# Kernel tuning notes

Hardware: AMD Instinct MI355X
Metric: run time of the kernel (lower is better)

Reference implementation:

```python
import jax, jax.numpy as jnp
import numpy as np

D_MODEL = 1024
H = 16
D_K = D_MODEL // H  # 64
B, S = 2, 2048


def setup_inputs() -> dict:
    key = jax.random.key(0)
    ks = jax.random.split(key, 8)
    scale = 1.0 / np.sqrt(D_MODEL)
    return {
        "q": jax.random.normal(ks[0], (B, S, D_MODEL), dtype=jnp.float32),
        "k": jax.random.normal(ks[1], (B, S, D_MODEL), dtype=jnp.float32),
        "v": jax.random.normal(ks[2], (B, S, D_MODEL), dtype=jnp.float32),
        "W_q": jax.random.normal(ks[3], (H, D_MODEL, D_K), dtype=jnp.float32) * scale,
        "W_k": jax.random.normal(ks[4], (H, D_MODEL, D_K), dtype=jnp.float32) * scale,
        "W_v": jax.random.normal(ks[5], (H, D_MODEL, D_K), dtype=jnp.float32) * scale,
        "W_o": jax.random.normal(ks[6], (D_MODEL, H * D_K), dtype=jnp.float32) * scale,
        "b_o": jnp.zeros((D_MODEL,), dtype=jnp.float32),
    }


def reference(q, k, v, W_q, W_k, W_v, W_o, b_o):
    b, s, _ = q.shape
    h, _, d_k = W_q.shape
    inv_sqrt_dk = jnp.asarray(1.0 / np.sqrt(d_k), q.dtype)
    # per-head projections: [b, h, s, d_k]
    qh = jnp.einsum("bsd,hdk->bhsk", q, W_q)
    kh = jnp.einsum("bsd,hdk->bhsk", k, W_k)
    vh = jnp.einsum("bsd,hdk->bhsk", v, W_v)
    # scaled dot product attention
    scores = jnp.einsum("bhqk,bhsk->bhqs", qh, kh) * inv_sqrt_dk  # [b,h,S,S]
    attn = jax.nn.softmax(scores, axis=-1)
    ctx = jnp.einsum("bhqs,bhsk->bhqk", attn, vh)  # [b,h,S,d_k]
    # chunk over heads + concat along feature dim -> [b, S, h*d_k], head-major
    ctx = ctx.transpose(0, 2, 1, 3).reshape(b, s, h * d_k)
    # final linear
    return ctx @ W_o.T + b_o
```

## Files before the change

kernel.cpp:

```cpp
#include <hip/hip_runtime.h>
#include <cstdint>
#include <cstddef>


typedef unsigned short bf16_t;
typedef __attribute__((ext_vector_type(8))) short short8;
typedef __attribute__((ext_vector_type(4))) float f32x4;

__device__ __forceinline__ uint32_t fbits(float f) {
  union { float f; uint32_t u; } v; v.f = f; return v.u;
}
__device__ __forceinline__ bf16_t f2bf(float f) {
  uint32_t u = fbits(f);
  return (bf16_t)((u + 0x7FFFu + ((u >> 16) & 1u)) >> 16);
}
__device__ __forceinline__ uint32_t packbf2(float lo, float hi) {
  uint32_t a = fbits(hi) + 0x8000u;
  uint32_t b = fbits(lo) + 0x8000u;
  return __builtin_amdgcn_perm(a, b, 0x07060302u);
}
__device__ __forceinline__ int4 cvt8(f32x4 lo, f32x4 hi) {
  return make_int4((int)packbf2(lo.x, lo.y), (int)packbf2(lo.z, lo.w),
                   (int)packbf2(hi.x, hi.y), (int)packbf2(hi.z, hi.w));
}

__global__ void prep_kernel(const float* __restrict__ Wo,
                            const float* __restrict__ Wq, const float* __restrict__ Wk,
                            const float* __restrict__ Wv,
                            bf16_t* __restrict__ Woo,
                            bf16_t* __restrict__ Wtq, bf16_t* __restrict__ Wtk,
                            bf16_t* __restrict__ Wtv) {
  int blk = blockIdx.x;
  int tid = threadIdx.x;
  if (blk < 1024) {
    int i = blk * 256 + tid;
    f32x4 val = ((const f32x4*)Wo)[i];
    ushort4 o;
    o.x = f2bf(val.x); o.y = f2bf(val.y); o.z = f2bf(val.z); o.w = f2bf(val.w);
    ((ushort4*)Woo)[i] = o;
  } else {
    int blk2 = blk - 1024;
    int z = blk2 >> 9, t = blk2 & 511;
    const float* W = z == 0 ? Wq : z == 1 ? Wk : Wv;
    bf16_t* Wt = z == 0 ? Wtq : z == 1 ? Wtk : Wtv;
    int h = t >> 5, d0 = (t & 31) * 32;
    __shared__ float tile[32][65];
    const float* src = W + ((size_t)h << 16) + (size_t)d0 * 64;
    int d = tid >> 3;
#pragma unroll
    for (int j = 0; j < 2; j++) {
      int dk = (tid & 7) * 8 + j * 4;
      *(f32x4*)&tile[d][dk] = *(const f32x4*)(src + d * 64 + dk);
    }
    __syncthreads();
    int dk2 = tid >> 2, c = tid & 3;
    union { ushort s[8]; int4 v; } o;
#pragma unroll
    for (int j = 0; j < 8; j++) o.s[j] = f2bf(tile[c * 8 + j][dk2]);
    *(int4*)(Wt + (size_t)(h * 64 + dk2) * 1024 + d0 + c * 8) = o.v;
  }
}

__global__ __launch_bounds__(256) void gemm_proj_kernel(
    const float* __restrict__ A0, const float* __restrict__ A1, const float* __restrict__ A2,
    const bf16_t* __restrict__ B0, const bf16_t* __restrict__ B1, const bf16_t* __restrict__ B2,
    bf16_t* __restrict__ O0, bf16_t* __restrict__ O1, bf16_t* __restrict__ O2,
    float s0)
{
  const int bid = blockIdx.x;
  const int nIdx = bid / 96;
  const int g = bid - nIdx * 96;
  const int z = g % 3;
  const int m0 = (g / 3) * 128, n0 = nIdx * 128;

  const float* A   = z == 0 ? A0 : z == 1 ? A1 : A2;
  const bf16_t* Bt = z == 0 ? B0 : z == 1 ? B1 : B2;
  bf16_t* Cout     = z == 0 ? O0 : z == 1 ? O1 : O2;
  const float scale = z == 0 ? s0 : 1.0f;
  const int K = 1024;

  __shared__ alignas(16) bf16_t smem[18432];

  const int tid = threadIdx.x;
  const int lane = tid & 63, wave = tid >> 6;
  const int wm = wave >> 1, wn = wave & 1;
  const int quad = lane >> 4, l15 = lane & 15;

  f32x4 acc[4][4];
#pragma unroll
  for (int i = 0; i < 4; i++)
#pragma unroll
    for (int j = 0; j < 4; j++) acc[i][j] = (f32x4)0.0f;

  const int c0 = wave * 128 + lane;
  const int c1 = c0 + 64;
  const float*  pa0 = A  + (size_t)(m0 + (c0 >> 2)) * K + (c0 & 3) * 8;
  const float*  pa1 = A  + (size_t)(m0 + (c1 >> 2)) * K + (c1 & 3) * 8;
  const bf16_t* pb0 = Bt + (size_t)(n0 + (c0 >> 2)) * K + (c0 & 3) * 8;
  const bf16_t* pb1 = Bt + (size_t)(n0 + (c1 >> 2)) * K + (c1 & 3) * 8;
  const int s0a = c0 * 8, s1a = c1 * 8;

  f32x4 ra0l = *(const f32x4*)pa0, ra0h = *(const f32x4*)(pa0 + 4);
  f32x4 ra1l = *(const f32x4*)pa1, ra1h = *(const f32x4*)(pa1 + 4);
  int4 rb0 = *(const int4*)pb0;
  int4 rb1 = *(const int4*)pb1;
  *(int4*)(smem + s0a) = cvt8(ra0l, ra0h);
  *(int4*)(smem + s1a) = cvt8(ra1l, ra1h);
  *(int4*)(smem + 4096 + s0a) = rb0;
  *(int4*)(smem + 4096 + s1a) = rb1;
  __syncthreads();

  for (int it = 0; it < 32; ++it) {
    const int co = (it & 1) * 8192;
    if (it < 31) {
      const int ko = (it + 1) * 32;
      ra0l = *(const f32x4*)(pa0 + ko); ra0h = *(const f32x4*)(pa0 + ko + 4);
      ra1l = *(const f32x4*)(pa1 + ko); ra1h = *(const f32x4*)(pa1 + ko + 4);
      rb0 = *(const int4*)(pb0 + ko);
      rb1 = *(const int4*)(pb1 + ko);
    }

    short8 af[4], bfr[4];
#pragma unroll
    for (int mi = 0; mi < 4; mi++)
      af[mi] = *(const short8*)(smem + co + (wm * 64 + mi * 16 + l15) * 32 + quad * 8);
#pragma unroll
    for (int ni = 0; ni < 4; ni++)
      bfr[ni] = *(const short8*)(smem + co + 4096 + (wn * 64 + ni * 16 + l15) * 32 + quad * 8);
#pragma unroll
    for (int mi = 0; mi < 4; mi++)
#pragma unroll
      for (int ni = 0; ni < 4; ni++)
        acc[mi][ni] = __builtin_amdgcn_mfma_f32_16x16x32_bf16(af[mi], bfr[ni], acc[mi][ni], 0, 0, 0);

    if (it < 31) {
      const int no = ((it + 1) & 1) * 8192;
      *(int4*)(smem + no + s0a) = cvt8(ra0l, ra0h);
      *(int4*)(smem + no + s1a) = cvt8(ra1l, ra1h);
      *(int4*)(smem + no + 4096 + s0a) = rb0;
      *(int4*)(smem + no + 4096 + s1a) = rb1;
    }
    __syncthreads();
  }

  const int s0r = m0 & 2047, bb = m0 >> 11, hp = n0 >> 6;
  if (z < 2) {
    bf16_t* slot = smem + wn * 9216;
#pragma unroll
    for (int ni = 0; ni < 4; ni++)
#pragma unroll
      for (int mi = 0; mi < 4; mi++)
#pragma unroll
        for (int r = 0; r < 4; r++)
          slot[(wm * 64 + mi * 16 + quad * 4 + r) * 72 + ni * 16 + l15] =
              f2bf(acc[mi][ni][r] * scale);
    __syncthreads();
#pragma unroll
    for (int rd = 0; rd < 8; ++rd) {
      int idx = rd * 256 + tid;
      int si = idx >> 10, mm = (idx >> 3) & 127, c8 = idx & 7;
      int4 val = *(const int4*)(smem + si * 9216 + mm * 72 + c8 * 8);
      *(int4*)(Cout + ((size_t)((bb * 16 + hp + si) * 2048 + s0r + mm)) * 64 + c8 * 8) = val;
    }
  } else {
    bf16_t* slot = smem + wn * 8704;
#pragma unroll
    for (int ni = 0; ni < 4; ni++)
#pragma unroll
      for (int mi = 0; mi < 4; mi++) {
        uint2 pk = make_uint2(packbf2(acc[mi][ni][0], acc[mi][ni][1]),
                              packbf2(acc[mi][ni][2], acc[mi][ni][3]));
        *(uint2*)(slot + (ni * 16 + l15) * 136 + wm * 64 + mi * 16 + quad * 4) = pk;
      }
    __syncthreads();
#pragma unroll
    for (int rd = 0; rd < 8; ++rd) {
      int idx = rd * 256 + tid;
      int si = idx >> 10, c = (idx >> 4) & 63, ck = idx & 15;
      int4 val = *(const int4*)(smem + si * 8704 + c * 136 + ck * 8);
      *(int4*)(Cout + (size_t)(bb * 16 + hp + si) * 131072 + (size_t)c * 2048 + s0r + ck * 8) = val;
    }
  }
}

__global__ __launch_bounds__(256) void gemm_out_kernel(
    const bf16_t* __restrict__ A, const bf16_t* __restrict__ Bt,
    float* __restrict__ C, const float* __restrict__ bias)
{
  const int K = 1024, N = 1024;
  __shared__ alignas(16) bf16_t smem[12288];
  const int tid = threadIdx.x;
  const int lane = tid & 63, wave = tid >> 6;
  const int quad = lane >> 4, l15 = lane & 15;
  const int m0 = (blockIdx.x & 31) * 128, n0 = (blockIdx.x >> 5) * 64;

  f32x4 acc[2][4];
#pragma unroll
  for (int i = 0; i < 2; i++)
#pragma unroll
    for (int j = 0; j < 4; j++) acc[i][j] = (f32x4)0.0f;

  const int c0 = wave * 128 + lane, c1 = c0 + 64;
  const int cb = wave * 64 + lane;
  const bf16_t* pa0 = A  + (size_t)(m0 + (c0 >> 2)) * K + (c0 & 3) * 8;
  const bf16_t* pa1 = A  + (size_t)(m0 + (c1 >> 2)) * K + (c1 & 3) * 8;
  const bf16_t* pb  = Bt + (size_t)(n0 + (cb >> 2)) * K + (cb & 3) * 8;
  const int s0a = c0 * 8, s1a = c1 * 8, sba = cb * 8;

  int4 ra0 = *(const int4*)pa0;
  int4 ra1 = *(const int4*)pa1;
  int4 rb  = *(const int4*)pb;
  *(int4*)(smem + s0a) = ra0;
  *(int4*)(smem + s1a) = ra1;
  *(int4*)(smem + 4096 + sba) = rb;
  __syncthreads();

  for (int it = 0; it < 32; ++it) {
    const int co = (it & 1) * 6144;
    if (it < 31) {
      const int ko = (it + 1) * 32;
      ra0 = *(const int4*)(pa0 + ko);
      ra1 = *(const int4*)(pa1 + ko);
      rb  = *(const int4*)(pb + ko);
    }

    short8 af[2], bfr[4];
#pragma unroll
    for (int mi = 0; mi < 2; mi++)
      af[mi] = *(const short8*)(smem + co + (wave * 32 + mi * 16 + l15) * 32 + quad * 8);
#pragma unroll
    for (int ni = 0; ni < 4; ni++)
      bfr[ni] = *(const short8*)(smem + co + 4096 + (ni * 16 + l15) * 32 + quad * 8);
#pragma unroll
    for (int mi = 0; mi < 2; mi++)
#pragma unroll
      for (int ni = 0; ni < 4; ni++)
        acc[mi][ni] = __builtin_amdgcn_mfma_f32_16x16x32_bf16(af[mi], bfr[ni], acc[mi][ni], 0, 0, 0);

    if (it < 31) {
      const int no = ((it + 1) & 1) * 6144;
      *(int4*)(smem + no + s0a) = ra0;
      *(int4*)(smem + no + s1a) = ra1;
      *(int4*)(smem + no + 4096 + sba) = rb;
    }
    __syncthreads();
  }

#pragma unroll
  for (int ni = 0; ni < 4; ni++) {
    int col = n0 + ni * 16 + l15;
    float bv = bias[col];
#pragma unroll
    for (int mi = 0; mi < 2; mi++) {
      int row = m0 + wave * 32 + mi * 16 + quad * 4;
#pragma unroll
      for (int r = 0; r < 4; r++)
        C[(size_t)(row + r) * N + col] = acc[mi][ni][r] + bv;
    }
  }
}

__global__ __launch_bounds__(512) void flash_kernel(
    const bf16_t* __restrict__ qh, const bf16_t* __restrict__ kh,
    const bf16_t* __restrict__ vT, bf16_t* __restrict__ ctx)
{
  __shared__ alignas(16) bf16_t KtF[2][4096];
  __shared__ alignas(16) bf16_t VtF[2][4096];
  __shared__ alignas(16) bf16_t PtF[16384];
  const int tid = threadIdx.x, lane = tid & 63, wave = tid >> 6;
  const int quad = lane >> 4, l15 = lane & 15;
  const int q0 = blockIdx.x * 256;
  const int h = blockIdx.y, b = blockIdx.z;
  const size_t headoff = (size_t)(b * 16 + h) * 2048 * 64;
  const bf16_t* Q = qh + headoff;
  const bf16_t* K = kh + headoff;
  const bf16_t* V = vT + headoff;

  short8 qf[2][2];
#pragma unroll
  for (int g = 0; g < 2; g++)
#pragma unroll
    for (int ks = 0; ks < 2; ks++)
      qf[g][ks] = *(const short8*)(Q + (size_t)(q0 + wave * 32 + g * 16 + l15) * 64
                                   + ks * 32 + quad * 8);

  f32x4 O[2][4];
#pragma unroll
  for (int g = 0; g < 2; g++)
#pragma unroll
    for (int mi = 0; mi < 4; mi++) O[g][mi] = (f32x4)0.0f;
  f32x4 lacc[2] = {(f32x4)0.0f, (f32x4)0.0f};

  const bf16_t* Kp = K + (size_t)((wave >> 1) * 16 + l15) * 64 + (wave & 1) * 32 + quad * 8;
  const bf16_t* Vp = V + (size_t)((wave >> 1) * 16 + l15) * 2048 + (wave & 1) * 32 + quad * 8;
  const int soff = wave * 512 + lane * 8;
  const int pwb = wave * 4096 + ((quad >> 1) * 16 + l15) * 16 + 8 * (quad & 1);

  auto body = [&](int buf) {
    f32x4 S[2][4];
#pragma unroll
    for (int g = 0; g < 2; g++)
#pragma unroll
      for (int mi = 0; mi < 4; mi++) S[g][mi] = (f32x4)0.0f;
#pragma unroll
    for (int ks = 0; ks < 2; ks++) {
#pragma unroll
      for (int mi = 0; mi < 4; mi++) {
        short8 kf = *(const short8*)(&KtF[buf][(mi * 2 + ks) * 512 + lane * 8]);
        S[0][mi] = __builtin_amdgcn_mfma_f32_16x16x32_bf16(kf, qf[0][ks], S[0][mi], 0, 0, 0);
        S[1][mi] = __builtin_amdgcn_mfma_f32_16x16x32_bf16(kf, qf[1][ks], S[1][mi], 0, 0, 0);
      }
    }
#pragma unroll
    for (int g = 0; g < 2; g++) {
#pragma unroll
      for (int mi = 0; mi < 4; mi++)
#pragma unroll
        for (int r = 0; r < 4; r++)
          S[g][mi][r] = __builtin_amdgcn_exp2f(S[g][mi][r]);
      lacc[g] += (S[g][0] + S[g][1]) + (S[g][2] + S[g][3]);
    }
#pragma unroll
    for (int g = 0; g < 2; g++)
#pragma unroll
      for (int mi = 0; mi < 4; mi++) {
        uint2 pk = make_uint2(packbf2(S[g][mi][0], S[g][mi][1]),
                              packbf2(S[g][mi][2], S[g][mi][3]));
        *(uint2*)((char*)PtF + pwb + g * 2048 + (mi >> 1) * 1024 + (mi & 1) * 512) = pk;
      }
#pragma unroll
    for (int ks = 0; ks < 2; ks++) {
      short8 pf0 = *(const short8*)(&PtF[wave * 2048 + (ks * 64 + lane) * 8]);
      short8 pf1 = *(const short8*)(&PtF[wave * 2048 + 1024 + (ks * 64 + lane) * 8]);
#pragma unroll
      for (int mi = 0; mi < 4; mi++) {
        short8 vf = *(const short8*)(&VtF[buf][(mi * 2 + ks) * 512 + lane * 8]);
        O[0][mi] = __builtin_amdgcn_mfma_f32_16x16x32_bf16(vf, pf0, O[0][mi], 0, 0, 0);
        O[1][mi] = __builtin_amdgcn_mfma_f32_16x16x32_bf16(vf, pf1, O[1][mi], 0, 0, 0);
      }
    }
  };

  int4 k0 = *(const int4*)Kp, v0 = *(const int4*)Vp;
  *(int4*)(&KtF[0][soff]) = k0;
  *(int4*)(&VtF[0][soff]) = v0;
  int4 kA = *(const int4*)(Kp + 4096), vA = *(const int4*)(Vp + 64);
  __syncthreads();

  for (int it = 0; it < 32; it += 2) {
    *(int4*)(&KtF[1][soff]) = kA;
    *(int4*)(&VtF[1][soff]) = vA;
    int4 kB, vB;
    if (it + 2 < 32) {
      kB = *(const int4*)(Kp + (size_t)(it + 2) * 4096);
      vB = *(const int4*)(Vp + (size_t)(it + 2) * 64);
    }
    body(0);
    __syncthreads();

    if (it + 2 < 32) {
      *(int4*)(&KtF[0][soff]) = kB;
      *(int4*)(&VtF[0][soff]) = vB;
    }
    if (it + 3 < 32) {
      kA = *(const int4*)(Kp + (size_t)(it + 3) * 4096);
      vA = *(const int4*)(Vp + (size_t)(it + 3) * 64);
    }
    body(1);
    __syncthreads();
  }

#pragma unroll
  for (int g = 0; g < 2; g++) {
    float l = (lacc[g][0] + lacc[g][1]) + (lacc[g][2] + lacc[g][3]);
    l += __shfl_xor(l, 16, 64);
    l += __shfl_xor(l, 32, 64);
    float inv = 1.0f / l;
    int qrow = q0 + wave * 32 + g * 16 + l15;
    bf16_t* crow = ctx + ((size_t)(b * 2048 + qrow)) * 1024 + h * 64;
#pragma unroll
    for (int mi = 0; mi < 4; mi++) {
      uint2 pk = make_uint2(packbf2(O[g][mi][0] * inv, O[g][mi][1] * inv),
                            packbf2(O[g][mi][2] * inv, O[g][mi][3] * inv));
      *(uint2*)(crow + mi * 16 + quad * 4) = pk;
    }
  }
}

extern "C" void kernel_launch(void* const* d_in, const int* in_sizes, int n_in,
                              void* d_out, int out_size, void* d_ws, size_t ws_size,
                              hipStream_t stream)
{
  const float* q  = (const float*)d_in[0];
  const float* k  = (const float*)d_in[1];
  const float* v  = (const float*)d_in[2];
  const float* Wq = (const float*)d_in[3];
  const float* Wk = (const float*)d_in[4];
  const float* Wv = (const float*)d_in[5];
  const float* Wo = (const float*)d_in[6];
  const float* bo = (const float*)d_in[7];
  float* out = (float*)d_out;

  const size_t NX = (size_t)4096 * 1024;
  const size_t NW = (size_t)1024 * 1024;

  char* p = (char*)d_ws;
  bf16_t* Wtq = (bf16_t*)p; p += NW * 2;
  bf16_t* Wtk = (bf16_t*)p; p += NW * 2;
  bf16_t* Wtv = (bf16_t*)p; p += NW * 2;
  bf16_t* Wob = (bf16_t*)p; p += NW * 2;
  bf16_t* qhb = (bf16_t*)p; p += NX * 2;
  bf16_t* khb = (bf16_t*)p; p += NX * 2;
  bf16_t* vTb = (bf16_t*)p; p += NX * 2;
  bf16_t* ctxb = (bf16_t*)p; p += NX * 2;

  prep_kernel<<<2560, 256, 0, stream>>>(Wo, Wq, Wk, Wv, Wob, Wtq, Wtk, Wtv);

  const float qscale = 0.125f * 1.44269504088896340736f;
  gemm_proj_kernel<<<768, 256, 0, stream>>>(q, k, v, Wtq, Wtk, Wtv,
                                            qhb, khb, vTb, qscale);

  flash_kernel<<<dim3(8, 16, 2), 512, 0, stream>>>(qhb, khb, vTb, ctxb);

  gemm_out_kernel<<<512, 256, 0, stream>>>(ctxb, Wob, out, bo);

  (void)in_sizes; (void)n_in; (void)out_size; (void)ws_size;
}
```

Measured before the change: 209.6 us.

## Deepen GEMM prefetch to two stages and enlarge output GEMM tile

Both the projection GEMM and the output GEMM now issue global loads two k-steps ahead, in a manually unrolled ping-pong loop, so load latency has a full compute step to hide behind. The output GEMM also moves from 128x64 tiles with 256 threads to 128x128 tiles with 512 threads in a 4x2 wave grid, which halves the grid to 256 blocks and increases reuse of each B tile. The cost is more live registers for the prefetched data and fewer blocks for the output GEMM, which may lower occupancy or leave some CUs idle.

Measured after the change: 219.5 us. 4.7% more time.

```diff
diff --git a/kernel.cpp b/kernel.cpp
--- a/kernel.cpp
+++ b/kernel.cpp
@@ -100,26 +100,7 @@
   const bf16_t* pb1 = Bt + (size_t)(n0 + (c1 >> 2)) * K + (c1 & 3) * 8;
   const int s0a = c0 * 8, s1a = c1 * 8;
 
-  f32x4 ra0l = *(const f32x4*)pa0, ra0h = *(const f32x4*)(pa0 + 4);
-  f32x4 ra1l = *(const f32x4*)pa1, ra1h = *(const f32x4*)(pa1 + 4);
-  int4 rb0 = *(const int4*)pb0;
-  int4 rb1 = *(const int4*)pb1;
-  *(int4*)(smem + s0a) = cvt8(ra0l, ra0h);
-  *(int4*)(smem + s1a) = cvt8(ra1l, ra1h);
-  *(int4*)(smem + 4096 + s0a) = rb0;
-  *(int4*)(smem + 4096 + s1a) = rb1;
-  __syncthreads();
-
-  for (int it = 0; it < 32; ++it) {
-    const int co = (it & 1) * 8192;
-    if (it < 31) {
-      const int ko = (it + 1) * 32;
-      ra0l = *(const f32x4*)(pa0 + ko); ra0h = *(const f32x4*)(pa0 + ko + 4);
-      ra1l = *(const f32x4*)(pa1 + ko); ra1h = *(const f32x4*)(pa1 + ko + 4);
-      rb0 = *(const int4*)(pb0 + ko);
-      rb1 = *(const int4*)(pb1 + ko);
-    }
-
+  auto compute = [&](int co) {
     short8 af[4], bfr[4];
 #pragma unroll
     for (int mi = 0; mi < 4; mi++)
@@ -132,14 +113,52 @@
 #pragma unroll
       for (int ni = 0; ni < 4; ni++)
         acc[mi][ni] = __builtin_amdgcn_mfma_f32_16x16x32_bf16(af[mi], bfr[ni], acc[mi][ni], 0, 0, 0);
-
-    if (it < 31) {
-      const int no = ((it + 1) & 1) * 8192;
-      *(int4*)(smem + no + s0a) = cvt8(ra0l, ra0h);
-      *(int4*)(smem + no + s1a) = cvt8(ra1l, ra1h);
-      *(int4*)(smem + no + 4096 + s0a) = rb0;
-      *(int4*)(smem + no + 4096 + s1a) = rb1;
-    }
+  };
+
+  {
+    f32x4 t0l = *(const f32x4*)pa0, t0h = *(const f32x4*)(pa0 + 4);
+    f32x4 t1l = *(const f32x4*)pa1, t1h = *(const f32x4*)(pa1 + 4);
+    *(int4*)(smem + s0a) = cvt8(t0l, t0h);
+    *(int4*)(smem + s1a) = cvt8(t1l, t1h);
+    *(int4*)(smem + 4096 + s0a) = *(const int4*)pb0;
+    *(int4*)(smem + 4096 + s1a) = *(const int4*)pb1;
+  }
+  f32x4 aA0l = *(const f32x4*)(pa0 + 32), aA0h = *(const f32x4*)(pa0 + 36);
+  f32x4 aA1l = *(const f32x4*)(pa1 + 32), aA1h = *(const f32x4*)(pa1 + 36);
+  int4  bA0  = *(const int4*)(pb0 + 32);
+  int4  bA1  = *(const int4*)(pb1 + 32);
+  __syncthreads();
+
+  f32x4 aB0l, aB0h, aB1l, aB1h; int4 bB0, bB1;
+  for (int it = 0; it < 32; it += 2) {
+    *(int4*)(smem + 8192 + s0a) = cvt8(aA0l, aA0h);
+    *(int4*)(smem + 8192 + s1a) = cvt8(aA1l, aA1h);
+    *(int4*)(smem + 8192 + 4096 + s0a) = bA0;
+    *(int4*)(smem + 8192 + 4096 + s1a) = bA1;
+    if (it + 2 < 32) {
+      const int ko = (it + 2) * 32;
+      aB0l = *(const f32x4*)(pa0 + ko); aB0h = *(const f32x4*)(pa0 + ko + 4);
+      aB1l = *(const f32x4*)(pa1 + ko); aB1h = *(const f32x4*)(pa1 + ko + 4);
+      bB0 = *(const int4*)(pb0 + ko);
+      bB1 = *(const int4*)(pb1 + ko);
+    }
+    compute(0);
+    __syncthreads();
+
+    if (it + 2 < 32) {
+      *(int4*)(smem + s0a) = cvt8(aB0l, aB0h);
+      *(int4*)(smem + s1a) = cvt8(aB1l, aB1h);
+      *(int4*)(smem + 4096 + s0a) = bB0;
+      *(int4*)(smem + 4096 + s1a) = bB1;
+    }
+    if (it + 3 < 32) {
+      const int ko = (it + 3) * 32;
+      aA0l = *(const f32x4*)(pa0 + ko); aA0h = *(const f32x4*)(pa0 + ko + 4);
+      aA1l = *(const f32x4*)(pa1 + ko); aA1h = *(const f32x4*)(pa1 + ko + 4);
+      bA0 = *(const int4*)(pb0 + ko);
+      bA1 = *(const int4*)(pb1 + ko);
+    }
+    compute(8192);
     __syncthreads();
   }
 
@@ -183,16 +202,17 @@
   }
 }
 
-__global__ __launch_bounds__(256) void gemm_out_kernel(
+__global__ __launch_bounds__(512) void gemm_out_kernel(
     const bf16_t* __restrict__ A, const bf16_t* __restrict__ Bt,
     float* __restrict__ C, const float* __restrict__ bias)
 {
   const int K = 1024, N = 1024;
-  __shared__ alignas(16) bf16_t smem[12288];
+  __shared__ alignas(16) bf16_t smem[16384];
   const int tid = threadIdx.x;
   const int lane = tid & 63, wave = tid >> 6;
+  const int wm = wave >> 1, wn = wave & 1;
   const int quad = lane >> 4, l15 = lane & 15;
-  const int m0 = (blockIdx.x & 31) * 128, n0 = (blockIdx.x >> 5) * 64;
+  const int m0 = (blockIdx.x & 31) * 128, n0 = (blockIdx.x >> 5) * 128;
 
   f32x4 acc[2][4];
 #pragma unroll
@@ -200,59 +220,65 @@
 #pragma unroll
     for (int j = 0; j < 4; j++) acc[i][j] = (f32x4)0.0f;
 
-  const int c0 = wave * 128 + lane, c1 = c0 + 64;
-  const int cb = wave * 64 + lane;
-  const bf16_t* pa0 = A  + (size_t)(m0 + (c0 >> 2)) * K + (c0 & 3) * 8;
-  const bf16_t* pa1 = A  + (size_t)(m0 + (c1 >> 2)) * K + (c1 & 3) * 8;
-  const bf16_t* pb  = Bt + (size_t)(n0 + (cb >> 2)) * K + (cb & 3) * 8;
-  const int s0a = c0 * 8, s1a = c1 * 8, sba = cb * 8;
-
-  int4 ra0 = *(const int4*)pa0;
-  int4 ra1 = *(const int4*)pa1;
-  int4 rb  = *(const int4*)pb;
-  *(int4*)(smem + s0a) = ra0;
-  *(int4*)(smem + s1a) = ra1;
-  *(int4*)(smem + 4096 + sba) = rb;
-  __syncthreads();
-
-  for (int it = 0; it < 32; ++it) {
-    const int co = (it & 1) * 6144;
-    if (it < 31) {
-      const int ko = (it + 1) * 32;
-      ra0 = *(const int4*)(pa0 + ko);
-      ra1 = *(const int4*)(pa1 + ko);
-      rb  = *(const int4*)(pb + ko);
-    }
-
+  const int ca = tid;
+  const int cb = tid;
+  const bf16_t* pa = A  + (size_t)(m0 + (ca >> 2)) * K + (ca & 3) * 8;
+  const bf16_t* pb = Bt + (size_t)(n0 + (cb >> 2)) * K + (cb & 3) * 8;
+  const int sa = ca * 8, sb = 4096 + cb * 8;
+
+  auto compute = [&](int co) {
     short8 af[2], bfr[4];
 #pragma unroll
     for (int mi = 0; mi < 2; mi++)
-      af[mi] = *(const short8*)(smem + co + (wave * 32 + mi * 16 + l15) * 32 + quad * 8);
+      af[mi] = *(const short8*)(smem + co + (wm * 32 + mi * 16 + l15) * 32 + quad * 8);
 #pragma unroll
     for (int ni = 0; ni < 4; ni++)
-      bfr[ni] = *(const short8*)(smem + co + 4096 + (ni * 16 + l15) * 32 + quad * 8);
+      bfr[ni] = *(const short8*)(smem + co + 4096 + (wn * 64 + ni * 16 + l15) * 32 + quad * 8);
 #pragma unroll
     for (int mi = 0; mi < 2; mi++)
 #pragma unroll
       for (int ni = 0; ni < 4; ni++)
         acc[mi][ni] = __builtin_amdgcn_mfma_f32_16x16x32_bf16(af[mi], bfr[ni], acc[mi][ni], 0, 0, 0);
-
-    if (it < 31) {
-      const int no = ((it + 1) & 1) * 6144;
-      *(int4*)(smem + no + s0a) = ra0;
-      *(int4*)(smem + no + s1a) = ra1;
-      *(int4*)(smem + no + 4096 + sba) = rb;
-    }
+  };
+
+  *(int4*)(smem + sa) = *(const int4*)pa;
+  *(int4*)(smem + sb) = *(const int4*)pb;
+  int4 rAa = *(const int4*)(pa + 32);
+  int4 rAb = *(const int4*)(pb + 32);
+  __syncthreads();
+
+  int4 rBa, rBb;
+  for (int it = 0; it < 32; it += 2) {
+    *(int4*)(smem + 8192 + sa) = rAa;
+    *(int4*)(smem + 8192 + sb) = rAb;
+    if (it + 2 < 32) {
+      const int ko = (it + 2) * 32;
+      rBa = *(const int4*)(pa + ko);
+      rBb = *(const int4*)(pb + ko);
+    }
+    compute(0);
+    __syncthreads();
+
+    if (it + 2 < 32) {
+      *(int4*)(smem + sa) = rBa;
+      *(int4*)(smem + sb) = rBb;
+    }
+    if (it + 3 < 32) {
+      const int ko = (it + 3) * 32;
+      rAa = *(const int4*)(pa + ko);
+      rAb = *(const int4*)(pb + ko);
+    }
+    compute(8192);
     __syncthreads();
   }
 
 #pragma unroll
   for (int ni = 0; ni < 4; ni++) {
-    int col = n0 + ni * 16 + l15;
+    int col = n0 + wn * 64 + ni * 16 + l15;
     float bv = bias[col];
 #pragma unroll
     for (int mi = 0; mi < 2; mi++) {
-      int row = m0 + wave * 32 + mi * 16 + quad * 4;
+      int row = m0 + wm * 32 + mi * 16 + quad * 4;
 #pragma unroll
       for (int r = 0; r < 4; r++)
         C[(size_t)(row + r) * N + col] = acc[mi][ni][r] + bv;
@@ -422,7 +448,7 @@
 
   flash_kernel<<<dim3(8, 16, 2), 512, 0, stream>>>(qhb, khb, vTb, ctxb);
 
-  gemm_out_kernel<<<512, 256, 0, stream>>>(ctxb, Wob, out, bo);
+  gemm_out_kernel<<<256, 512, 0, stream>>>(ctxb, Wob, out, bo);
 
   (void)in_sizes; (void)n_in; (void)out_size; (void)ws_size;
 }
```
